# Kernel tuning notes

Hardware: AMD Instinct MI355X
Metric: run time of the kernel (lower is better)

## Reference

```python
import jax, jax.numpy as jnp
import numpy as np

DIM = 1024
N_HEADS = 16
B, S = 2, 2048


def setup_inputs() -> dict:
    key = jax.random.key(0)
    ks = jax.random.split(key, 5)
    scale = 1.0 / np.sqrt(DIM)
    x = jax.random.normal(ks[0], (B, S, DIM), dtype=jnp.float32)
    mask = jax.random.randint(ks[1], (B, S), 0, 2, dtype=jnp.int32)
    Wq = jax.random.normal(ks[2], (DIM, DIM), dtype=jnp.float32) * scale
    Wk = jax.random.normal(ks[3], (DIM, DIM), dtype=jnp.float32) * scale
    Wv = jax.random.normal(ks[4], (DIM, DIM), dtype=jnp.float32) * scale
    bq = jnp.zeros((DIM,), jnp.float32)
    bk = jnp.zeros((DIM,), jnp.float32)
    bv = jnp.zeros((DIM,), jnp.float32)
    return {"x": x, "mask": mask, "Wq": Wq, "bq": bq, "Wk": Wk, "bk": bk, "Wv": Wv, "bv": bv}


def reference(x, mask, Wq, bq, Wk, bk, Wv, bv):
    # x: (B,S,D); project to q,k,v then split heads: (B,H,S,Dh)
    H = N_HEADS
    Bn, Sn, D = x.shape
    Dh = D // H

    def heads(t):
        return t.reshape(Bn, Sn, H, Dh).transpose(0, 2, 1, 3)

    q = heads(x @ Wq + bq)
    k = heads(x @ Wk + bk)
    v = heads(x @ Wv + bv)

    scores = jnp.einsum("bhsd,bhtd->bhst", q, k) / jnp.sqrt(jnp.float32(Dh))
    m = mask.astype(jnp.float32)[:, None, None, :]  # (B,1,1,S)
    scores = scores - 10000.0 * (1.0 - m)
    attn = jax.nn.softmax(scores, axis=-1)  # dropout is identity at eval (p=0)
    h = jnp.einsum("bhst,bhtd->bhsd", attn, v)
    return h.transpose(0, 2, 1, 3).reshape(Bn, Sn, D)
```

## Files before the change

### kernel.cpp

```cpp
#include <hip/hip_runtime.h>
#include <math.h>

#define DIMD 1024
#define NH 16
#define DH 64
#define BB 2
#define SS 2048
#define M_TOTAL (BB * SS)

typedef _Float16 half8 __attribute__((ext_vector_type(8)));
typedef _Float16 half4v __attribute__((ext_vector_type(4)));
typedef __fp16 fp16x2 __attribute__((ext_vector_type(2)));
typedef float floatx4 __attribute__((ext_vector_type(4)));
typedef float floatx16 __attribute__((ext_vector_type(16)));

#define QSCALE 0.18033688011112042f

__device__ __forceinline__ void load16_to_lds(const void* g, void* l) {
    __builtin_amdgcn_global_load_lds(
        (const __attribute__((address_space(1))) void*)g,
        (__attribute__((address_space(3))) void*)l, 16, 0, 0);
}

__global__ __launch_bounds__(64) void scan_mask_kernel(
    const int* __restrict__ mask, int* __restrict__ pos, int* __restrict__ nvalid)
{
    const int b = blockIdx.x, lane = threadIdx.x;
    int base = 0;
    const unsigned long long lanemask = (lane == 63)
        ? 0x7fffffffffffffffull : ((1ull << lane) - 1ull);
    for (int c = 0; c < SS / 64; ++c) {
        const int mv = mask[b * SS + c * 64 + lane];
        const unsigned long long bm = __ballot(mv != 0);
        const int pc = __popcll(bm & lanemask);
        pos[b * SS + c * 64 + lane] = mv ? (base + pc) : -1;
        base += __popcll(bm);
    }
    if (lane == 0) nvalid[b] = base;
}

__global__ __launch_bounds__(256) void cvt_x_kernel(
    const float* __restrict__ x, _Float16* __restrict__ xh)
{
    const int i = blockIdx.x * 256 + threadIdx.x;
    float4 v = ((const float4*)x)[i];
    half4v h = {(_Float16)v.x, (_Float16)v.y, (_Float16)v.z, (_Float16)v.w};
    *(half4v*)&xh[(size_t)i * 4] = h;
}

__global__ __launch_bounds__(256) void cvt_wt_kernel(
    const float* __restrict__ Wq, const float* __restrict__ Wk,
    const float* __restrict__ Wv, _Float16* __restrict__ Wt)
{
    const float* W = blockIdx.z == 0 ? Wq : (blockIdx.z == 1 ? Wk : Wv);
    _Float16* o = Wt + (size_t)blockIdx.z * DIMD * DIMD;
    __shared__ _Float16 Ls[32][34];
    const int k0 = blockIdx.x * 32, n0 = blockIdx.y * 32;
    const int tid = threadIdx.x;
    const int r = tid >> 3, c4 = (tid & 7) * 4;

    float4 v = *(const float4*)&W[(size_t)(k0 + r) * DIMD + n0 + c4];
    Ls[r][c4 + 0] = (_Float16)v.x;
    Ls[r][c4 + 1] = (_Float16)v.y;
    Ls[r][c4 + 2] = (_Float16)v.z;
    Ls[r][c4 + 3] = (_Float16)v.w;
    __syncthreads();

    half4v h = {Ls[c4 + 0][r], Ls[c4 + 1][r], Ls[c4 + 2][r], Ls[c4 + 3][r]};
    *(half4v*)&o[(size_t)(n0 + r) * DIMD + k0 + c4] = h;
}

__global__ __launch_bounds__(256) void proj_gemm(
    const _Float16* __restrict__ xh, const _Float16* __restrict__ Wt,
    const float* __restrict__ bq, const float* __restrict__ bk,
    const float* __restrict__ bv, const int* __restrict__ pos,
    _Float16* __restrict__ Q, _Float16* __restrict__ K, _Float16* __restrict__ Vt)
{
    const int z = blockIdx.z;
    const float* bias = z == 0 ? bq : (z == 1 ? bk : bv);
    const _Float16* Wz = Wt + (size_t)z * DIMD * DIMD;

    __shared__ _Float16 Ah[128 * 64];
    __shared__ _Float16 Bh[128 * 64];

    const int tid = threadIdx.x;
    const int wave = tid >> 6, lane = tid & 63;
    const int quad = lane >> 4, l16 = lane & 15;
    const int wm = (wave >> 1) * 64, wn = (wave & 1) * 64;
    const int m0 = blockIdx.x * 128, n0 = blockIdx.y * 128;
    const int sw = l16 & 7;

    floatx4 acc[4][4];
#pragma unroll
    for (int i = 0; i < 4; ++i)
#pragma unroll
        for (int j = 0; j < 4; ++j) acc[i][j] = (floatx4){0.f, 0.f, 0.f, 0.f};

    for (int k0 = 0; k0 < DIMD; k0 += 64) {
        __syncthreads();
#pragma unroll
        for (int it = 0; it < 4; ++it) {
            const int u = it * 256 + tid;
            const int row = u >> 3;
            const int gc = (u & 7) ^ (row & 7);
            load16_to_lds(&xh[(size_t)(m0 + row) * DIMD + k0 + gc * 8],
                          &Ah[(size_t)(it * 256 + wave * 64) * 8]);
        }
#pragma unroll
        for (int it = 0; it < 4; ++it) {
            const int u = it * 256 + tid;
            const int row = u >> 3;
            const int gc = (u & 7) ^ (row & 7);
            load16_to_lds(&Wz[(size_t)(n0 + row) * DIMD + k0 + gc * 8],
                          &Bh[(size_t)(it * 256 + wave * 64) * 8]);
        }
        __syncthreads();

#pragma unroll
        for (int kc = 0; kc < 2; ++kc) {
            const int coff = ((quad + kc * 4) ^ sw) * 8;
            half8 af[4], bf[4];
#pragma unroll
            for (int mt = 0; mt < 4; ++mt)
                af[mt] = *(const half8*)&Ah[(wm + mt * 16 + l16) * 64 + coff];
#pragma unroll
            for (int nt = 0; nt < 4; ++nt)
                bf[nt] = *(const half8*)&Bh[(wn + nt * 16 + l16) * 64 + coff];
#pragma unroll
            for (int mt = 0; mt < 4; ++mt)
#pragma unroll
                for (int nt = 0; nt < 4; ++nt)
                    acc[mt][nt] = __builtin_amdgcn_mfma_f32_16x16x32_f16(
                        af[mt], bf[nt], acc[mt][nt], 0, 0, 0);
        }
    }

    int prr[4][4], brow[4][4], srow[4][4];
#pragma unroll
    for (int mt = 0; mt < 4; ++mt)
#pragma unroll
        for (int r = 0; r < 4; ++r) {
            const int m = m0 + wm + mt * 16 + quad * 4 + r;
            brow[mt][r] = m >> 11;
            srow[mt][r] = m & 2047;
            prr[mt][r] = (z == 0) ? 0 : pos[m];
        }

#pragma unroll
    for (int nt = 0; nt < 4; ++nt) {
        const int n = n0 + wn + nt * 16 + l16;
        const float bn = bias[n];
        const int h = n >> 6, d = n & 63;
#pragma unroll
        for (int mt = 0; mt < 4; ++mt) {
#pragma unroll
            for (int r = 0; r < 4; ++r) {
                const int b = brow[mt][r];
                const _Float16 val = (_Float16)((acc[mt][nt][r] + bn) *
                                                (z == 0 ? QSCALE : 1.0f));
                if (z == 0) {
                    Q[((((size_t)b * NH + h) * SS + srow[mt][r]) << 6) + d] = val;
                } else if (prr[mt][r] >= 0) {
                    if (z == 1)
                        K[((((size_t)b * NH + h) * SS + prr[mt][r]) << 6) + d] = val;
                    else
                        Vt[(((size_t)b * NH + h) * DH + d) * SS + prr[mt][r]] = val;
                }
            }
        }
    }
}

__global__ __launch_bounds__(256, 2) void attn_kernel(
    const _Float16* __restrict__ Q, const _Float16* __restrict__ K,
    const _Float16* __restrict__ Vt, const int* __restrict__ nvalid,
    float* __restrict__ out)
{
    __shared__ __align__(16) char smem[34816];
    const int bh = blockIdx.y, b = bh >> 4, h = bh & 15;
    const int q0 = blockIdx.x * 128;
    const int tid = threadIdx.x, wave = tid >> 6, lane = tid & 63;
    const int hi = lane >> 5, l31 = lane & 31;

    const _Float16* Qb = Q + (size_t)bh * SS * DH;
    const _Float16* Kb = K + (size_t)bh * SS * DH;
    const _Float16* Vtb = Vt + (size_t)bh * DH * SS;

    const int nv = nvalid[b];
    const int ntiles = (nv + 63) >> 6;

    half8 qf[4];
#pragma unroll
    for (int ks = 0; ks < 4; ++ks)
        qf[ks] = *(const half8*)&Qb[(size_t)(q0 + wave * 32 + l31) * DH
                                    + ks * 16 + hi * 8];

#pragma unroll
    for (int it = 0; it < 2; ++it) {
        const int u = it * 256 + tid;
        const int row = u >> 3, gc = (u & 7) ^ (row & 7);
        load16_to_lds(&Kb[(size_t)row * DH + gc * 8],
                      (_Float16*)smem + (size_t)(it * 256 + wave * 64) * 8);
    }
#pragma unroll
    for (int it = 0; it < 2; ++it) {
        const int u = it * 256 + tid;
        const int row = u >> 3, gc = (u & 7) ^ (row & 7);
        load16_to_lds(&Vtb[(size_t)row * SS + gc * 8],
                      (_Float16*)(smem + 16384) + (size_t)(it * 256 + wave * 64) * 8);
    }
    __syncthreads();

    floatx16 O0, O1;
#pragma unroll
    for (int r = 0; r < 16; ++r) { O0[r] = 0.f; O1[r] = 0.f; }
    float m = -1e30f, l = 0.f;

    for (int i = 0; i < ntiles; ++i) {
        const int buf = i & 1;
        const int t0 = i * 64;

        if (i + 1 < ntiles) {
            const int nb = buf ^ 1, nt0 = t0 + 64;
            _Float16* KsN = (_Float16*)(smem + nb * 8192);
#pragma unroll
            for (int it = 0; it < 2; ++it) {
                const int u = it * 256 + tid;
                const int row = u >> 3, gc = (u & 7) ^ (row & 7);
                load16_to_lds(&Kb[(size_t)(nt0 + row) * DH + gc * 8],
                              KsN + (size_t)(it * 256 + wave * 64) * 8);
            }
            _Float16* VtN = (_Float16*)(smem + 16384 + nb * 8192);
#pragma unroll
            for (int it = 0; it < 2; ++it) {
                const int u = it * 256 + tid;
                const int row = u >> 3, gc = (u & 7) ^ (row & 7);
                load16_to_lds(&Vtb[(size_t)row * SS + nt0 + gc * 8],
                              VtN + (size_t)(it * 256 + wave * 64) * 8);
            }
        }

        const _Float16* KsB = (const _Float16*)(smem + buf * 8192);
        const _Float16* VtB = (const _Float16*)(smem + 16384 + buf * 8192);

        floatx16 S0, S1;
#pragma unroll
        for (int r = 0; r < 16; ++r) { S0[r] = 0.f; S1[r] = 0.f; }
#pragma unroll
        for (int ks = 0; ks < 4; ++ks) {
            const int c = 2 * ks + hi;
            const int r0 = l31, r1 = 32 + l31;
            half8 a0 = *(const half8*)&KsB[r0 * 64 + ((c ^ (r0 & 7)) << 3)];
            half8 a1 = *(const half8*)&KsB[r1 * 64 + ((c ^ (r1 & 7)) << 3)];
            S0 = __builtin_amdgcn_mfma_f32_32x32x16_f16(a0, qf[ks], S0, 0, 0, 0);
            S1 = __builtin_amdgcn_mfma_f32_32x32x16_f16(a1, qf[ks], S1, 0, 0, 0);
        }

        if (t0 + 64 > nv) {
#pragma unroll
            for (int r = 0; r < 16; ++r) {
                const int tr = (r & 3) + 8 * (r >> 2) + 4 * hi;
                S0[r] = (t0 + tr < nv) ? S0[r] : -1e30f;
                S1[r] = (t0 + 32 + tr < nv) ? S1[r] : -1e30f;
            }
        }

        float tmax = -1e30f;
#pragma unroll
        for (int r = 0; r < 16; ++r)
            tmax = fmaxf(tmax, fmaxf(S0[r], S1[r]));
        tmax = fmaxf(tmax, __shfl_xor(tmax, 32));
        const float mn = fmaxf(m, tmax);
        const float alpha = exp2f(m - mn);
        m = mn;

        float p0[16], p1[16];
        float lsum = 0.f;
#pragma unroll
        for (int r = 0; r < 16; ++r) {
            const float e0 = exp2f(S0[r] - m);
            const float e1 = exp2f(S1[r] - m);
            p0[r] = e0; p1[r] = e1;
            lsum += e0 + e1;
        }
        lsum += __shfl_xor(lsum, 32);
        l = l * alpha + lsum;
#pragma unroll
        for (int r = 0; r < 16; ++r) { O0[r] *= alpha; O1[r] *= alpha; }

        unsigned int pk0[8], pk1[8];
#pragma unroll
        for (int j = 0; j < 8; ++j) {
            union { fp16x2 hv; unsigned int u; } cv;
            cv.hv = __builtin_amdgcn_cvt_pkrtz(p0[2 * j], p0[2 * j + 1]);
            pk0[j] = cv.u;
            cv.hv = __builtin_amdgcn_cvt_pkrtz(p1[2 * j], p1[2 * j + 1]);
            pk1[j] = cv.u;
        }

#pragma unroll
        for (int ks = 0; ks < 4; ++ks) {
            const int k1 = ks & 1;
            const unsigned int* pk = (ks < 2) ? pk0 : pk1;
            const unsigned int a0 = pk[4 * k1 + 0], a1 = pk[4 * k1 + 1];
            const unsigned int b0 = pk[4 * k1 + 2], b1 = pk[4 * k1 + 3];
            const unsigned int s0 = hi ? a0 : b0, s1 = hi ? a1 : b1;
            const unsigned int r0v = __shfl_xor(s0, 32);
            const unsigned int r1v = __shfl_xor(s1, 32);
            union { unsigned int u[4]; half8 hv; } bf;
            bf.u[0] = hi ? r0v : a0;
            bf.u[1] = hi ? r1v : a1;
            bf.u[2] = hi ? b0 : r0v;
            bf.u[3] = hi ? b1 : r1v;
            const int c = 2 * ks + hi;
            const int rd0 = l31, rd1 = 32 + l31;
            half8 v0 = *(const half8*)&VtB[rd0 * 64 + ((c ^ (rd0 & 7)) << 3)];
            half8 v1 = *(const half8*)&VtB[rd1 * 64 + ((c ^ (rd1 & 7)) << 3)];
            O0 = __builtin_amdgcn_mfma_f32_32x32x16_f16(v0, bf.hv, O0, 0, 0, 0);
            O1 = __builtin_amdgcn_mfma_f32_32x32x16_f16(v1, bf.hv, O1, 0, 0, 0);
        }

        __syncthreads();
    }

    const float inv = 1.f / l;
    float* Ob = (float*)smem + wave * (32 * 68);
#pragma unroll
    for (int r = 0; r < 16; ++r) {
        const int dbase = (r & 3) + 8 * (r >> 2) + 4 * hi;
        Ob[l31 * 68 + dbase] = O0[r] * inv;
        Ob[l31 * 68 + 32 + dbase] = O1[r] * inv;
    }
    __syncthreads();

    const int qq = lane >> 1, part = lane & 1;
    float* op = out + ((size_t)(b * SS + q0 + wave * 32 + qq)) * DIMD
              + h * DH + part * 32;
#pragma unroll
    for (int j = 0; j < 8; ++j)
        *(float4*)&op[j * 4] = *(const float4*)&Ob[qq * 68 + part * 32 + j * 4];
}

extern "C" void kernel_launch(void* const* d_in, const int* in_sizes, int n_in,
                              void* d_out, int out_size, void* d_ws, size_t ws_size,
                              hipStream_t stream) {
    const float* x  = (const float*)d_in[0];
    const int* mask = (const int*)d_in[1];
    const float* Wq = (const float*)d_in[2];
    const float* bq = (const float*)d_in[3];
    const float* Wk = (const float*)d_in[4];
    const float* bk = (const float*)d_in[5];
    const float* Wv = (const float*)d_in[6];
    const float* bv = (const float*)d_in[7];
    float* out = (float*)d_out;

    _Float16* xh = (_Float16*)d_ws;
    _Float16* Wt = xh + (size_t)M_TOTAL * DIMD;
    _Float16* Q  = Wt + (size_t)3 * DIMD * DIMD;
    _Float16* K  = Q + (size_t)M_TOTAL * DIMD;
    _Float16* Vt = K + (size_t)M_TOTAL * DIMD;
    int* pos     = (int*)(Vt + (size_t)M_TOTAL * DIMD);
    int* nvalid  = pos + M_TOTAL;

    scan_mask_kernel<<<BB, 64, 0, stream>>>(mask, pos, nvalid);
    cvt_x_kernel<<<M_TOTAL * DIMD / 1024, 256, 0, stream>>>(x, xh);
    cvt_wt_kernel<<<dim3(32, 32, 3), 256, 0, stream>>>(Wq, Wk, Wv, Wt);
    proj_gemm<<<dim3(M_TOTAL / 128, DIMD / 128, 3), 256, 0, stream>>>(
        xh, Wt, bq, bk, bv, pos, Q, K, Vt);
    attn_kernel<<<dim3(SS / 128, BB * NH), 256, 0, stream>>>(Q, K, Vt, nvalid, out);
}
```

Baseline: 181.4 us.

## Fuse prep kernels, double-buffer projection GEMM, swap operands for coalesced V^T stores

Result: slower. 191.5 us (+5.6%).

```diff
diff --git a/kernel.cpp b/kernel.cpp
--- a/kernel.cpp
+++ b/kernel.cpp
@@ -22,52 +22,69 @@
         (__attribute__((address_space(3))) void*)l, 16, 0, 0);
 }
 
-__global__ __launch_bounds__(64) void scan_mask_kernel(
-    const int* __restrict__ mask, int* __restrict__ pos, int* __restrict__ nvalid)
+__global__ __launch_bounds__(256) void prep_kernel(
+    const float* __restrict__ x,
+    const float* __restrict__ Wq, const float* __restrict__ Wk,
+    const float* __restrict__ Wv, const int* __restrict__ mask,
+    _Float16* __restrict__ xh, _Float16* __restrict__ Wt,
+    int* __restrict__ pos, int* __restrict__ nvalid)
 {
-    const int b = blockIdx.x, lane = threadIdx.x;
-    int base = 0;
-    const unsigned long long lanemask = (lane == 63)
-        ? 0x7fffffffffffffffull : ((1ull << lane) - 1ull);
-    for (int c = 0; c < SS / 64; ++c) {
-        const int mv = mask[b * SS + c * 64 + lane];
-        const unsigned long long bm = __ballot(mv != 0);
-        const int pc = __popcll(bm & lanemask);
-        pos[b * SS + c * 64 + lane] = mv ? (base + pc) : -1;
-        base += __popcll(bm);
-    }
-    if (lane == 0) nvalid[b] = base;
-}
-
-__global__ __launch_bounds__(256) void cvt_x_kernel(
-    const float* __restrict__ x, _Float16* __restrict__ xh)
-{
-    const int i = blockIdx.x * 256 + threadIdx.x;
-    float4 v = ((const float4*)x)[i];
-    half4v h = {(_Float16)v.x, (_Float16)v.y, (_Float16)v.z, (_Float16)v.w};
-    *(half4v*)&xh[(size_t)i * 4] = h;
-}
-
-__global__ __launch_bounds__(256) void cvt_wt_kernel(
-    const float* __restrict__ Wq, const float* __restrict__ Wk,
-    const float* __restrict__ Wv, _Float16* __restrict__ Wt)
-{
-    const float* W = blockIdx.z == 0 ? Wq : (blockIdx.z == 1 ? Wk : Wv);
-    _Float16* o = Wt + (size_t)blockIdx.z * DIMD * DIMD;
     __shared__ _Float16 Ls[32][34];
-    const int k0 = blockIdx.x * 32, n0 = blockIdx.y * 32;
-    const int tid = threadIdx.x;
-    const int r = tid >> 3, c4 = (tid & 7) * 4;
-
-    float4 v = *(const float4*)&W[(size_t)(k0 + r) * DIMD + n0 + c4];
-    Ls[r][c4 + 0] = (_Float16)v.x;
-    Ls[r][c4 + 1] = (_Float16)v.y;
-    Ls[r][c4 + 2] = (_Float16)v.z;
-    Ls[r][c4 + 3] = (_Float16)v.w;
-    __syncthreads();
-
-    half4v h = {Ls[c4 + 0][r], Ls[c4 + 1][r], Ls[c4 + 2][r], Ls[c4 + 3][r]};
-    *(half4v*)&o[(size_t)(n0 + r) * DIMD + k0 + c4] = h;
+    __shared__ int cnt[32], off[32];
+    const int bid = blockIdx.x, tid = threadIdx.x;
+
+    if (bid < 1024) {
+#pragma unroll
+        for (int j = 0; j < 4; ++j) {
+            const int i = j * 262144 + bid * 256 + tid;
+            float4 v = ((const float4*)x)[i];
+            half4v hv = {(_Float16)v.x, (_Float16)v.y, (_Float16)v.z, (_Float16)v.w};
+            *(half4v*)&xh[(size_t)i * 4] = hv;
+        }
+    } else if (bid < 4096) {
+        const int wid = bid - 1024;
+        const int z = wid >> 10, rem = wid & 1023;
+        const float* W = z == 0 ? Wq : (z == 1 ? Wk : Wv);
+        _Float16* o = Wt + (size_t)z * DIMD * DIMD;
+        const int k0 = (rem >> 5) * 32, n0 = (rem & 31) * 32;
+        const int r = tid >> 3, c4 = (tid & 7) * 4;
+
+        float4 v = *(const float4*)&W[(size_t)(k0 + r) * DIMD + n0 + c4];
+        Ls[r][c4 + 0] = (_Float16)v.x;
+        Ls[r][c4 + 1] = (_Float16)v.y;
+        Ls[r][c4 + 2] = (_Float16)v.z;
+        Ls[r][c4 + 3] = (_Float16)v.w;
+        __syncthreads();
+        half4v h = {Ls[c4 + 0][r], Ls[c4 + 1][r], Ls[c4 + 2][r], Ls[c4 + 3][r]};
+        *(half4v*)&o[(size_t)(n0 + r) * DIMD + k0 + c4] = h;
+    } else {
+        const int b = bid - 4096;
+        const int wv = tid >> 6, lane = tid & 63;
+        const unsigned long long lanemask = (lane == 63)
+            ? 0x7fffffffffffffffull : ((1ull << lane) - 1ull);
+        unsigned long long bms[8];
+#pragma unroll
+        for (int cc = 0; cc < 8; ++cc) {
+            const int c = wv * 8 + cc;
+            const int mv = mask[b * SS + c * 64 + lane];
+            bms[cc] = __ballot(mv != 0);
+            if (lane == 0) cnt[c] = __popcll(bms[cc]);
+        }
+        __syncthreads();
+        if (tid == 0) {
+            int s = 0;
+            for (int c = 0; c < 32; ++c) { off[c] = s; s += cnt[c]; }
+            nvalid[b] = s;
+        }
+        __syncthreads();
+#pragma unroll
+        for (int cc = 0; cc < 8; ++cc) {
+            const int c = wv * 8 + cc;
+            const int valid = (int)((bms[cc] >> lane) & 1ull);
+            pos[b * SS + c * 64 + lane] =
+                valid ? (off[c] + __popcll(bms[cc] & lanemask)) : -1;
+        }
+    }
 }
 
 __global__ __launch_bounds__(256) void proj_gemm(
@@ -80,15 +97,17 @@
     const float* bias = z == 0 ? bq : (z == 1 ? bk : bv);
     const _Float16* Wz = Wt + (size_t)z * DIMD * DIMD;
 
-    __shared__ _Float16 Ah[128 * 64];
-    __shared__ _Float16 Bh[128 * 64];
+    const _Float16* Aptr; const _Float16* Bptr; int m0, n0;
+    if (z == 2) { Aptr = Wz; Bptr = xh; m0 = blockIdx.y * 128; n0 = blockIdx.x * 128; }
+    else        { Aptr = xh; Bptr = Wz; m0 = blockIdx.x * 128; n0 = blockIdx.y * 128; }
+
+    __shared__ _Float16 Ah[2][128 * 32];
+    __shared__ _Float16 Bh[2][128 * 32];
 
     const int tid = threadIdx.x;
     const int wave = tid >> 6, lane = tid & 63;
     const int quad = lane >> 4, l16 = lane & 15;
     const int wm = (wave >> 1) * 64, wn = (wave & 1) * 64;
-    const int m0 = blockIdx.x * 128, n0 = blockIdx.y * 128;
-    const int sw = l16 & 7;
 
     floatx4 acc[4][4];
 #pragma unroll
@@ -96,75 +115,97 @@
 #pragma unroll
         for (int j = 0; j < 4; ++j) acc[i][j] = (floatx4){0.f, 0.f, 0.f, 0.f};
 
-    for (int k0 = 0; k0 < DIMD; k0 += 64) {
+    auto stage = [&](int buf, int k0) {
+#pragma unroll
+        for (int it = 0; it < 2; ++it) {
+            const int u = it * 256 + tid;
+            const int row = u >> 2;
+            const int gc = (u & 3) ^ ((row >> 1) & 3);
+            load16_to_lds(&Aptr[(size_t)(m0 + row) * DIMD + k0 + gc * 8],
+                          &Ah[buf][(size_t)(it * 256 + wave * 64) * 8]);
+        }
+#pragma unroll
+        for (int it = 0; it < 2; ++it) {
+            const int u = it * 256 + tid;
+            const int row = u >> 2;
+            const int gc = (u & 3) ^ ((row >> 1) & 3);
+            load16_to_lds(&Bptr[(size_t)(n0 + row) * DIMD + k0 + gc * 8],
+                          &Bh[buf][(size_t)(it * 256 + wave * 64) * 8]);
+        }
+    };
+
+    stage(0, 0);
+    __syncthreads();
+
+    for (int kt = 0; kt < 32; ++kt) {
+        if (kt + 1 < 32) stage((kt + 1) & 1, (kt + 1) * 32);
+
+        const _Float16* A = Ah[kt & 1];
+        const _Float16* B = Bh[kt & 1];
+        half8 af[4], bf[4];
+#pragma unroll
+        for (int mt = 0; mt < 4; ++mt) {
+            const int row = wm + mt * 16 + l16;
+            af[mt] = *(const half8*)&A[row * 32 + ((quad ^ ((row >> 1) & 3)) << 3)];
+        }
+#pragma unroll
+        for (int nt = 0; nt < 4; ++nt) {
+            const int row = wn + nt * 16 + l16;
+            bf[nt] = *(const half8*)&B[row * 32 + ((quad ^ ((row >> 1) & 3)) << 3)];
+        }
+#pragma unroll
+        for (int mt = 0; mt < 4; ++mt)
+#pragma unroll
+            for (int nt = 0; nt < 4; ++nt)
+                acc[mt][nt] = __builtin_amdgcn_mfma_f32_16x16x32_f16(
+                    af[mt], bf[nt], acc[mt][nt], 0, 0, 0);
+
         __syncthreads();
-#pragma unroll
-        for (int it = 0; it < 4; ++it) {
-            const int u = it * 256 + tid;
-            const int row = u >> 3;
-            const int gc = (u & 7) ^ (row & 7);
-            load16_to_lds(&xh[(size_t)(m0 + row) * DIMD + k0 + gc * 8],
-                          &Ah[(size_t)(it * 256 + wave * 64) * 8]);
-        }
-#pragma unroll
-        for (int it = 0; it < 4; ++it) {
-            const int u = it * 256 + tid;
-            const int row = u >> 3;
-            const int gc = (u & 7) ^ (row & 7);
-            load16_to_lds(&Wz[(size_t)(n0 + row) * DIMD + k0 + gc * 8],
-                          &Bh[(size_t)(it * 256 + wave * 64) * 8]);
-        }
-        __syncthreads();
-
-#pragma unroll
-        for (int kc = 0; kc < 2; ++kc) {
-            const int coff = ((quad + kc * 4) ^ sw) * 8;
-            half8 af[4], bf[4];
-#pragma unroll
-            for (int mt = 0; mt < 4; ++mt)
-                af[mt] = *(const half8*)&Ah[(wm + mt * 16 + l16) * 64 + coff];
-#pragma unroll
-            for (int nt = 0; nt < 4; ++nt)
-                bf[nt] = *(const half8*)&Bh[(wn + nt * 16 + l16) * 64 + coff];
-#pragma unroll
-            for (int mt = 0; mt < 4; ++mt)
-#pragma unroll
-                for (int nt = 0; nt < 4; ++nt)
-                    acc[mt][nt] = __builtin_amdgcn_mfma_f32_16x16x32_f16(
-                        af[mt], bf[nt], acc[mt][nt], 0, 0, 0);
-        }
-    }
-
-    int prr[4][4], brow[4][4], srow[4][4];
-#pragma unroll
-    for (int mt = 0; mt < 4; ++mt)
-#pragma unroll
-        for (int r = 0; r < 4; ++r) {
-            const int m = m0 + wm + mt * 16 + quad * 4 + r;
-            brow[mt][r] = m >> 11;
-            srow[mt][r] = m & 2047;
-            prr[mt][r] = (z == 0) ? 0 : pos[m];
-        }
-
-#pragma unroll
-    for (int nt = 0; nt < 4; ++nt) {
-        const int n = n0 + wn + nt * 16 + l16;
-        const float bn = bias[n];
-        const int h = n >> 6, d = n & 63;
-#pragma unroll
-        for (int mt = 0; mt < 4; ++mt) {
+    }
+
+    if (z < 2) {
+        int prr[4][4];
+#pragma unroll
+        for (int mt = 0; mt < 4; ++mt)
 #pragma unroll
             for (int r = 0; r < 4; ++r) {
-                const int b = brow[mt][r];
-                const _Float16 val = (_Float16)((acc[mt][nt][r] + bn) *
-                                                (z == 0 ? QSCALE : 1.0f));
-                if (z == 0) {
-                    Q[((((size_t)b * NH + h) * SS + srow[mt][r]) << 6) + d] = val;
-                } else if (prr[mt][r] >= 0) {
-                    if (z == 1)
-                        K[((((size_t)b * NH + h) * SS + prr[mt][r]) << 6) + d] = val;
-                    else
-                        Vt[(((size_t)b * NH + h) * DH + d) * SS + prr[mt][r]] = val;
+                const int m = m0 + wm + mt * 16 + quad * 4 + r;
+                prr[mt][r] = (z == 0) ? (m & 2047) : pos[m];
+            }
+#pragma unroll
+        for (int nt = 0; nt < 4; ++nt) {
+            const int n = n0 + wn + nt * 16 + l16;
+            const float bn = bias[n];
+            const int h = n >> 6, d = n & 63;
+#pragma unroll
+            for (int mt = 0; mt < 4; ++mt) {
+#pragma unroll
+                for (int r = 0; r < 4; ++r) {
+                    if (prr[mt][r] < 0) continue;
+                    const int m = m0 + wm + mt * 16 + quad * 4 + r;
+                    const int b = m >> 11;
+                    const _Float16 val = (_Float16)((acc[mt][nt][r] + bn) *
+                                                    (z == 0 ? QSCALE : 1.0f));
+                    _Float16* dst = (z == 0) ? Q : K;
+                    dst[((((size_t)b * NH + h) * SS + prr[mt][r]) << 6) + d] = val;
+                }
+            }
+        }
+    } else {
+#pragma unroll
+        for (int nt = 0; nt < 4; ++nt) {
+            const int gs = n0 + wn + nt * 16 + l16;
+            const int prn = pos[gs];
+            const int b = gs >> 11;
+#pragma unroll
+            for (int mt = 0; mt < 4; ++mt) {
+#pragma unroll
+                for (int r = 0; r < 4; ++r) {
+                    if (prn < 0) continue;
+                    const int drow = m0 + wm + mt * 16 + quad * 4 + r;
+                    const int h = drow >> 6, dh = drow & 63;
+                    Vt[(((size_t)b * NH + h) * DH + dh) * SS + prn] =
+                        (_Float16)(acc[mt][nt][r] + bias[drow]);
                 }
             }
         }
@@ -307,17 +348,17 @@
             const unsigned int s0 = hi ? a0 : b0, s1 = hi ? a1 : b1;
             const unsigned int r0v = __shfl_xor(s0, 32);
             const unsigned int r1v = __shfl_xor(s1, 32);
-            union { unsigned int u[4]; half8 hv; } bf;
-            bf.u[0] = hi ? r0v : a0;
-            bf.u[1] = hi ? r1v : a1;
-            bf.u[2] = hi ? b0 : r0v;
-            bf.u[3] = hi ? b1 : r1v;
+            union { unsigned int u[4]; half8 hv; } bfu;
+            bfu.u[0] = hi ? r0v : a0;
+            bfu.u[1] = hi ? r1v : a1;
+            bfu.u[2] = hi ? b0 : r0v;
+            bfu.u[3] = hi ? b1 : r1v;
             const int c = 2 * ks + hi;
             const int rd0 = l31, rd1 = 32 + l31;
             half8 v0 = *(const half8*)&VtB[rd0 * 64 + ((c ^ (rd0 & 7)) << 3)];
             half8 v1 = *(const half8*)&VtB[rd1 * 64 + ((c ^ (rd1 & 7)) << 3)];
-            O0 = __builtin_amdgcn_mfma_f32_32x32x16_f16(v0, bf.hv, O0, 0, 0, 0);
-            O1 = __builtin_amdgcn_mfma_f32_32x32x16_f16(v1, bf.hv, O1, 0, 0, 0);
+            O0 = __builtin_amdgcn_mfma_f32_32x32x16_f16(v0, bfu.hv, O0, 0, 0, 0);
+            O1 = __builtin_amdgcn_mfma_f32_32x32x16_f16(v1, bfu.hv, O1, 0, 0, 0);
         }
 
         __syncthreads();
@@ -362,10 +403,8 @@
     int* pos     = (int*)(Vt + (size_t)M_TOTAL * DIMD);
     int* nvalid  = pos + M_TOTAL;
 
-    scan_mask_kernel<<<BB, 64, 0, stream>>>(mask, pos, nvalid);
-    cvt_x_kernel<<<M_TOTAL * DIMD / 1024, 256, 0, stream>>>(x, xh);
-    cvt_wt_kernel<<<dim3(32, 32, 3), 256, 0, stream>>>(Wq, Wk, Wv, Wt);
-    proj_gemm<<<dim3(M_TOTAL / 128, DIMD / 128, 3), 256, 0, stream>>>(
+    prep_kernel<<<4098, 256, 0, stream>>>(x, Wq, Wk, Wv, mask, xh, Wt, pos, nvalid);
+    proj_gemm<<<dim3(32, 8, 3), 256, 0, stream>>>(
         xh, Wt, bq, bk, bv, pos, Q, K, Vt);
     attn_kernel<<<dim3(SS / 128, BB * NH), 256, 0, stream>>>(Q, K, Vt, nvalid, out);
 }
```
